# Optimization experiments

Measured on AMD Instinct MI355X. Metric: run time of the kernel, lower is better.

The kernel has to match this reference:

```python
import jax, jax.numpy as jnp
import numpy as np

TQ, TV, TA = 40, 64, 40
B = 2048
D = 1280          # per-stream feature dim; 4*D == 10*EMBED
EMBED = 512
EPS = 1e-5


def setup_inputs() -> dict:
    key = jax.random.key(0)
    ks = jax.random.split(key, 10)
    q  = jax.random.normal(ks[0], (TQ, B, D), jnp.float32)
    vq = jax.random.normal(ks[1], (TV, B, D), jnp.float32)
    a  = jax.random.normal(ks[2], (TA, B, D), jnp.float32)
    va = jax.random.normal(ks[3], (TV, B, D), jnp.float32)
    qlen = jax.random.randint(ks[4], (B,), 1, TQ + 1, dtype=jnp.int32)
    alen = jax.random.randint(ks[5], (B,), 1, TA + 1, dtype=jnp.int32)
    # classifier params (xavier-ish init)
    W1 = jax.random.normal(ks[6], (4 * D, EMBED), jnp.float32) * (2.0 / (4 * D + EMBED)) ** 0.5
    b1 = jnp.zeros((EMBED,), jnp.float32)
    gamma = jnp.ones((EMBED,), jnp.float32)
    beta = jnp.zeros((EMBED,), jnp.float32)
    W2 = jax.random.normal(ks[7], (EMBED, 1), jnp.float32) * (2.0 / (EMBED + 1)) ** 0.5
    b2 = jnp.zeros((1,), jnp.float32)
    return dict(question_embedding_v=q, visual_embedding_qu=vq,
                answer_embedding_v_expand=a, visual_embedding_an_expand=va,
                W1=W1, b1=b1, gamma=gamma, beta=beta, W2=W2, b2=b2,
                question_len=qlen, answers_len=alen)


def _masked_mean(x, lens):
    # x: [T, B, D], lens: [B] -> mean over first lens[j] timesteps per sample -> [B, D]
    T = x.shape[0]
    mask = (jnp.arange(T)[:, None] < lens[None, :]).astype(x.dtype)  # [T, B]
    return jnp.einsum('tbd,tb->bd', x, mask) / lens.astype(x.dtype)[:, None]


def reference(question_embedding_v, visual_embedding_qu,
              answer_embedding_v_expand, visual_embedding_an_expand,
              W1, b1, gamma, beta, W2, b2,
              question_len, answers_len):
    q  = _masked_mean(question_embedding_v, question_len)          # [B, D]
    vq = visual_embedding_qu.mean(axis=0)                          # [B, D]
    a  = _masked_mean(answer_embedding_v_expand, answers_len)      # [B, D]
    va = visual_embedding_an_expand.mean(axis=0)                   # [B, D]
    feat = jnp.concatenate([q, vq, a, va], axis=1)                 # [B, 4D] = [B, 10*EMBED]
    # Dropout is identity in eval/reference; BatchNorm1d uses batch stats (training mode).
    h = jax.nn.elu(feat @ W1 + b1)                                 # [B, EMBED]
    mu = h.mean(axis=0)
    var = h.var(axis=0)                                            # biased, like torch BN
    h = (h - mu) * jax.lax.rsqrt(var + EPS) * gamma + beta
    return h @ W2 + b2                                             # [B, 1]
```

## Files before the change

kernel.cpp:

```cpp
#include <hip/hip_runtime.h>
#include <hip/hip_bf16.h>

typedef __attribute__((ext_vector_type(8))) short bf16x8;
typedef __attribute__((ext_vector_type(4))) float f32x4;

#define NB 2048
#define ND 1280
#define NK 5120
#define NE 512

static __device__ inline unsigned short f2bf(float x) {
    union { float f; unsigned u; } c; c.f = x;
    unsigned r = c.u + 0x7FFFu + ((c.u >> 16) & 1u);
    return (unsigned short)(r >> 16);
}

__global__ __launch_bounds__(256) void reduce_kernel(
    const float4* __restrict__ q, const float4* __restrict__ vq,
    const float4* __restrict__ aa, const float4* __restrict__ va,
    const int* __restrict__ qlen, const int* __restrict__ alen,
    ushort4* __restrict__ feat)
{
    const int tid = blockIdx.x * 256 + threadIdx.x;
    const int per_seg = NB * (ND / 4);
    const int seg = tid / per_seg;
    const int r = tid - seg * per_seg;
    const int b = r / (ND / 4);
    const int ch = r - b * (ND / 4);

    const float4* src;
    int len;
    if (seg == 0)      { src = q;  len = qlen[b]; }
    else if (seg == 1) { src = vq; len = 64; }
    else if (seg == 2) { src = aa; len = alen[b]; }
    else               { src = va; len = 64; }

    const long base = (long)b * (ND / 4) + ch;
    const long stride = (long)NB * (ND / 4);

    float4 acc = make_float4(0.f, 0.f, 0.f, 0.f);
    #pragma unroll 4
    for (int t = 0; t < len; ++t) {
        float4 v = src[base + (long)t * stride];
        acc.x += v.x; acc.y += v.y; acc.z += v.z; acc.w += v.w;
    }
    const float inv = 1.0f / (float)len;
    ushort4 o;
    o.x = f2bf(acc.x * inv);
    o.y = f2bf(acc.y * inv);
    o.z = f2bf(acc.z * inv);
    o.w = f2bf(acc.w * inv);
    feat[(long)b * (NK / 4) + seg * (ND / 4) + ch] = o;
}

__global__ __launch_bounds__(256) void w1t_kernel(
    const float* __restrict__ W1, unsigned short* __restrict__ w1t)
{
    __shared__ unsigned short lds[32][33];
    const int bid = blockIdx.x;
    const int kb = (bid >> 4) * 32;
    const int nb = (bid & 15) * 32;
    const int tx = threadIdx.x & 31;
    const int ty = threadIdx.x >> 5;
    #pragma unroll
    for (int i = 0; i < 4; ++i) {
        int k = kb + ty + i * 8;
        lds[ty + i * 8][tx] = f2bf(W1[(long)k * NE + nb + tx]);
    }
    __syncthreads();
    #pragma unroll
    for (int i = 0; i < 4; ++i) {
        int n = nb + ty + i * 8;
        w1t[(long)n * NK + kb + tx] = lds[tx][ty + i * 8];
    }
}

__global__ __launch_bounds__(256) void gemm_kernel(
    const unsigned short* __restrict__ feat, const unsigned short* __restrict__ w1t,
    float* __restrict__ hpart)
{
    __shared__ int4 As[64 * 9];
    __shared__ int4 Bs[64 * 9];

    const int bid = blockIdx.x;
    const int tile = bid & 255;
    const int s = bid >> 8;
    const int m0 = (tile >> 3) << 6;
    const int n0 = (tile & 7) << 6;
    const int kbeg = s * (NK / 4);

    const int t = threadIdx.x;
    const int l = t & 63;
    const int w = t >> 6;
    const int wm = (w >> 1) * 32;
    const int wn = (w & 1) * 32;
    const int srow = t >> 3;
    const int scol = t & 7;

    f32x4 acc[2][2] = {};

    for (int k0 = kbeg; k0 < kbeg + NK / 4; k0 += 64) {
        const unsigned short* Ag = feat + (long)(m0 + srow) * NK + k0 + scol * 8;
        const unsigned short* Bg = w1t + (long)(n0 + srow) * NK + k0 + scol * 8;
        int4 a0 = *(const int4*)Ag;
        int4 a1 = *(const int4*)(Ag + 32L * NK);
        int4 b0 = *(const int4*)Bg;
        int4 b1v = *(const int4*)(Bg + 32L * NK);
        As[srow * 9 + scol] = a0;
        As[(srow + 32) * 9 + scol] = a1;
        Bs[srow * 9 + scol] = b0;
        Bs[(srow + 32) * 9 + scol] = b1v;
        __syncthreads();
        #pragma unroll
        for (int kk = 0; kk < 2; ++kk) {
            const int kc = kk * 4 + (l >> 4);
            bf16x8 af0 = *(const bf16x8*)&As[(wm + (l & 15)) * 9 + kc];
            bf16x8 af1 = *(const bf16x8*)&As[(wm + 16 + (l & 15)) * 9 + kc];
            bf16x8 bf0 = *(const bf16x8*)&Bs[(wn + (l & 15)) * 9 + kc];
            bf16x8 bf1 = *(const bf16x8*)&Bs[(wn + 16 + (l & 15)) * 9 + kc];
            acc[0][0] = __builtin_amdgcn_mfma_f32_16x16x32_bf16(af0, bf0, acc[0][0], 0, 0, 0);
            acc[0][1] = __builtin_amdgcn_mfma_f32_16x16x32_bf16(af0, bf1, acc[0][1], 0, 0, 0);
            acc[1][0] = __builtin_amdgcn_mfma_f32_16x16x32_bf16(af1, bf0, acc[1][0], 0, 0, 0);
            acc[1][1] = __builtin_amdgcn_mfma_f32_16x16x32_bf16(af1, bf1, acc[1][1], 0, 0, 0);
        }
        __syncthreads();
    }

    float* hp = hpart + (long)s * NB * NE;
    const int rbase = m0 + wm + ((l >> 4) << 2);
    const int cbase = n0 + wn + (l & 15);
    #pragma unroll
    for (int mi = 0; mi < 2; ++mi)
        #pragma unroll
        for (int ni = 0; ni < 2; ++ni)
            #pragma unroll
            for (int rr = 0; rr < 4; ++rr)
                hp[(long)(rbase + mi * 16 + rr) * NE + cbase + ni * 16] = acc[mi][ni][rr];
}

__global__ __launch_bounds__(256) void combine_kernel(
    const float* __restrict__ hpart, const float* __restrict__ b1,
    float* __restrict__ h, float* __restrict__ part1, float* __restrict__ part2)
{
    const int blk = blockIdx.x;
    const int t = threadIdx.x;
    const int c = t * 2;
    const float bx = b1[c], by = b1[c + 1];
    float s1x = 0.f, s1y = 0.f, s2x = 0.f, s2y = 0.f;
    const float2* hp = (const float2*)hpart;
    float2* h2 = (float2*)h;
    const long SL = (long)NB * NE / 2;
    for (int i = 0; i < 32; ++i) {
        long row = (long)blk * 32 + i;
        long idx = row * (NE / 2) + t;
        float2 v0 = hp[idx];
        float2 v1 = hp[idx + SL];
        float2 v2 = hp[idx + 2 * SL];
        float2 v3 = hp[idx + 3 * SL];
        float hx = v0.x + v1.x + v2.x + v3.x + bx;
        float hy = v0.y + v1.y + v2.y + v3.y + by;
        hx = hx > 0.f ? hx : expm1f(hx);
        hy = hy > 0.f ? hy : expm1f(hy);
        h2[idx] = make_float2(hx, hy);
        s1x += hx; s2x += hx * hx;
        s1y += hy; s2y += hy * hy;
    }
    float2* p1 = (float2*)part1;
    float2* p2 = (float2*)part2;
    p1[blk * (NE / 2) + t] = make_float2(s1x, s1y);
    p2[blk * (NE / 2) + t] = make_float2(s2x, s2y);
}

__global__ __launch_bounds__(512) void finalize_kernel(
    const float* __restrict__ part1, const float* __restrict__ part2,
    const float* __restrict__ gamma, const float* __restrict__ beta,
    const float* __restrict__ W2, const float* __restrict__ b2,
    float* __restrict__ coefA, float* __restrict__ cst)
{
    const int e = threadIdx.x;
    float s1 = 0.f, s2 = 0.f;
    for (int i = 0; i < 64; ++i) {
        s1 += part1[i * NE + e];
        s2 += part2[i * NE + e];
    }
    const float mu = s1 * (1.0f / NB);
    const float var = s2 * (1.0f / NB) - mu * mu;
    const float rs = rsqrtf(var + 1e-5f);
    const float g = gamma[e], w = W2[e];
    coefA[e] = rs * g * w;
    float term = (beta[e] - mu * rs * g) * w;
    __shared__ float red[512];
    red[e] = term;
    __syncthreads();
    for (int off = 256; off > 0; off >>= 1) {
        if (e < off) red[e] += red[e + off];
        __syncthreads();
    }
    if (e == 0) cst[0] = red[0] + b2[0];
}

__global__ __launch_bounds__(256) void out_kernel(
    const float* __restrict__ h, const float* __restrict__ coefA,
    const float* __restrict__ cst, float* __restrict__ out)
{
    const int w = threadIdx.x >> 6;
    const int l = threadIdx.x & 63;
    const int row = blockIdx.x * 4 + w;
    const float4* h4 = (const float4*)(h + (long)row * NE);
    const float4* c4 = (const float4*)coefA;
    float4 x0 = h4[l * 2], x1 = h4[l * 2 + 1];
    float4 c0 = c4[l * 2], c1 = c4[l * 2 + 1];
    float dot = x0.x * c0.x + x0.y * c0.y + x0.z * c0.z + x0.w * c0.w
              + x1.x * c1.x + x1.y * c1.y + x1.z * c1.z + x1.w * c1.w;
    #pragma unroll
    for (int off = 32; off > 0; off >>= 1) dot += __shfl_down(dot, off);
    if (l == 0) out[row] = dot + cst[0];
}

extern "C" void kernel_launch(void* const* d_in, const int* in_sizes, int n_in,
                              void* d_out, int out_size, void* d_ws, size_t ws_size,
                              hipStream_t stream)
{
    const float* q    = (const float*)d_in[0];
    const float* vq   = (const float*)d_in[1];
    const float* aa   = (const float*)d_in[2];
    const float* va   = (const float*)d_in[3];
    const float* W1   = (const float*)d_in[4];
    const float* b1   = (const float*)d_in[5];
    const float* gam  = (const float*)d_in[6];
    const float* bet  = (const float*)d_in[7];
    const float* W2   = (const float*)d_in[8];
    const float* b2   = (const float*)d_in[9];
    const int* qlen   = (const int*)d_in[10];
    const int* alen   = (const int*)d_in[11];
    float* out = (float*)d_out;

    char* ws = (char*)d_ws;
    unsigned short* feat = (unsigned short*)ws;
    unsigned short* w1t  = (unsigned short*)(ws + 20971520);
    float* hbuf          = (float*)(ws + 26214400);
    float* hpart         = (float*)(ws + 30408704);
    float* part1         = (float*)(ws + 47185920);
    float* part2         = (float*)(ws + 47316992);
    float* coefA         = (float*)(ws + 47448064);
    float* cst           = (float*)(ws + 47450112);

    reduce_kernel<<<10240, 256, 0, stream>>>(
        (const float4*)q, (const float4*)vq, (const float4*)aa, (const float4*)va,
        qlen, alen, (ushort4*)feat);

    w1t_kernel<<<2560, 256, 0, stream>>>(W1, w1t);

    gemm_kernel<<<1024, 256, 0, stream>>>(feat, w1t, hpart);

    combine_kernel<<<64, 256, 0, stream>>>(hpart, b1, hbuf, part1, part2);

    finalize_kernel<<<1, 512, 0, stream>>>(part1, part2, gam, bet, W2, b2, coefA, cst);

    out_kernel<<<512, 256, 0, stream>>>(hbuf, coefA, cst, out);
}
```

Before: 392.8 us.

## Fuse BN finalize into output kernel, atomically accumulate stats, widen reduce per-thread work

The reduce kernel now has each thread accumulate two float4 columns, which halves the grid. It also fully specialises the fixed-length (64) visual streams so their loop can be unrolled. The combine kernel runs on 256 blocks of 8 rows instead of 64 blocks of 32 rows, and pushes its per-column sums and sums of squares into a global buffer with atomics. The w1t kernel zeroes that buffer beforehand. The single-block finalize kernel is removed, and every output block now recomputes the BN coefficients into LDS itself. This drops one launch and a serial single-block step, at the cost of redundant coefficient work per block and nondeterministic float atomic ordering.

```diff
diff --git a/kernel.cpp b/kernel.cpp
--- a/kernel.cpp
+++ b/kernel.cpp
@@ -22,40 +22,59 @@
     ushort4* __restrict__ feat)
 {
     const int tid = blockIdx.x * 256 + threadIdx.x;
-    const int per_seg = NB * (ND / 4);
+    const int per_seg = NB * 160;
     const int seg = tid / per_seg;
     const int r = tid - seg * per_seg;
-    const int b = r / (ND / 4);
-    const int ch = r - b * (ND / 4);
-
-    const float4* src;
-    int len;
-    if (seg == 0)      { src = q;  len = qlen[b]; }
-    else if (seg == 1) { src = vq; len = 64; }
-    else if (seg == 2) { src = aa; len = alen[b]; }
-    else               { src = va; len = 64; }
-
-    const long base = (long)b * (ND / 4) + ch;
-    const long stride = (long)NB * (ND / 4);
-
-    float4 acc = make_float4(0.f, 0.f, 0.f, 0.f);
-    #pragma unroll 4
-    for (int t = 0; t < len; ++t) {
-        float4 v = src[base + (long)t * stride];
-        acc.x += v.x; acc.y += v.y; acc.z += v.z; acc.w += v.w;
-    }
-    const float inv = 1.0f / (float)len;
-    ushort4 o;
-    o.x = f2bf(acc.x * inv);
-    o.y = f2bf(acc.y * inv);
-    o.z = f2bf(acc.z * inv);
-    o.w = f2bf(acc.w * inv);
-    feat[(long)b * (NK / 4) + seg * (ND / 4) + ch] = o;
+    const int b = r / 160;
+    const int ch = r - b * 160;
+
+    const long base = (long)b * 320 + ch;
+    const long stride = (long)NB * 320;
+
+    float4 a0 = make_float4(0.f, 0.f, 0.f, 0.f);
+    float4 a1 = make_float4(0.f, 0.f, 0.f, 0.f);
+    float inv;
+
+    if (seg == 1 || seg == 3) {
+        const float4* src = (seg == 1) ? vq : va;
+        #pragma unroll 8
+        for (int t = 0; t < 64; ++t) {
+            float4 v0 = src[base + (long)t * stride];
+            float4 v1 = src[base + 160 + (long)t * stride];
+            a0.x += v0.x; a0.y += v0.y; a0.z += v0.z; a0.w += v0.w;
+            a1.x += v1.x; a1.y += v1.y; a1.z += v1.z; a1.w += v1.w;
+        }
+        inv = 1.0f / 64.0f;
+    } else {
+        const float4* src = (seg == 0) ? q : aa;
+        const int len = (seg == 0) ? qlen[b] : alen[b];
+        #pragma unroll 4
+        for (int t = 0; t < len; ++t) {
+            float4 v0 = src[base + (long)t * stride];
+            float4 v1 = src[base + 160 + (long)t * stride];
+            a0.x += v0.x; a0.y += v0.y; a0.z += v0.z; a0.w += v0.w;
+            a1.x += v1.x; a1.y += v1.y; a1.z += v1.z; a1.w += v1.w;
+        }
+        inv = 1.0f / (float)len;
+    }
+
+    ushort4 o0, o1;
+    o0.x = f2bf(a0.x * inv); o0.y = f2bf(a0.y * inv);
+    o0.z = f2bf(a0.z * inv); o0.w = f2bf(a0.w * inv);
+    o1.x = f2bf(a1.x * inv); o1.y = f2bf(a1.y * inv);
+    o1.z = f2bf(a1.z * inv); o1.w = f2bf(a1.w * inv);
+    const long fb = (long)b * (NK / 4) + seg * 320 + ch;
+    feat[fb] = o0;
+    feat[fb + 160] = o1;
 }
 
 __global__ __launch_bounds__(256) void w1t_kernel(
-    const float* __restrict__ W1, unsigned short* __restrict__ w1t)
-{
+    const float* __restrict__ W1, unsigned short* __restrict__ w1t,
+    float* __restrict__ s1s2)
+{
+    if (blockIdx.x == 0) {
+        ((float4*)s1s2)[threadIdx.x] = make_float4(0.f, 0.f, 0.f, 0.f);
+    }
     __shared__ unsigned short lds[32][33];
     const int bid = blockIdx.x;
     const int kb = (bid >> 4) * 32;
@@ -140,7 +159,7 @@
 
 __global__ __launch_bounds__(256) void combine_kernel(
     const float* __restrict__ hpart, const float* __restrict__ b1,
-    float* __restrict__ h, float* __restrict__ part1, float* __restrict__ part2)
+    float* __restrict__ h, float* __restrict__ s1s2)
 {
     const int blk = blockIdx.x;
     const int t = threadIdx.x;
@@ -150,8 +169,9 @@
     const float2* hp = (const float2*)hpart;
     float2* h2 = (float2*)h;
     const long SL = (long)NB * NE / 2;
-    for (int i = 0; i < 32; ++i) {
-        long row = (long)blk * 32 + i;
+    #pragma unroll
+    for (int i = 0; i < 8; ++i) {
+        long row = (long)blk * 8 + i;
         long idx = row * (NE / 2) + t;
         float2 v0 = hp[idx];
         float2 v1 = hp[idx + SL];
@@ -165,56 +185,56 @@
         s1x += hx; s2x += hx * hx;
         s1y += hy; s2y += hy * hy;
     }
-    float2* p1 = (float2*)part1;
-    float2* p2 = (float2*)part2;
-    p1[blk * (NE / 2) + t] = make_float2(s1x, s1y);
-    p2[blk * (NE / 2) + t] = make_float2(s2x, s2y);
-}
-
-__global__ __launch_bounds__(512) void finalize_kernel(
-    const float* __restrict__ part1, const float* __restrict__ part2,
+    unsafeAtomicAdd(&s1s2[c], s1x);
+    unsafeAtomicAdd(&s1s2[c + 1], s1y);
+    unsafeAtomicAdd(&s1s2[NE + c], s2x);
+    unsafeAtomicAdd(&s1s2[NE + c + 1], s2y);
+}
+
+__global__ __launch_bounds__(256) void out_kernel(
+    const float* __restrict__ h, const float* __restrict__ s1s2,
     const float* __restrict__ gamma, const float* __restrict__ beta,
     const float* __restrict__ W2, const float* __restrict__ b2,
-    float* __restrict__ coefA, float* __restrict__ cst)
-{
-    const int e = threadIdx.x;
-    float s1 = 0.f, s2 = 0.f;
-    for (int i = 0; i < 64; ++i) {
-        s1 += part1[i * NE + e];
-        s2 += part2[i * NE + e];
-    }
-    const float mu = s1 * (1.0f / NB);
-    const float var = s2 * (1.0f / NB) - mu * mu;
-    const float rs = rsqrtf(var + 1e-5f);
-    const float g = gamma[e], w = W2[e];
-    coefA[e] = rs * g * w;
-    float term = (beta[e] - mu * rs * g) * w;
-    __shared__ float red[512];
-    red[e] = term;
+    float* __restrict__ out)
+{
+    __shared__ float coef[NE];
+    __shared__ float red[256];
+    const int t = threadIdx.x;
+
+    float term = 0.f;
+    #pragma unroll
+    for (int i = 0; i < 2; ++i) {
+        const int e = t + i * 256;
+        const float s1 = s1s2[e];
+        const float s2 = s1s2[NE + e];
+        const float mu = s1 * (1.0f / NB);
+        const float var = s2 * (1.0f / NB) - mu * mu;
+        const float rs = rsqrtf(var + 1e-5f);
+        const float g = gamma[e], wv = W2[e];
+        coef[e] = rs * g * wv;
+        term += (beta[e] - mu * rs * g) * wv;
+    }
+    red[t] = term;
     __syncthreads();
-    for (int off = 256; off > 0; off >>= 1) {
-        if (e < off) red[e] += red[e + off];
+    #pragma unroll
+    for (int off = 128; off > 0; off >>= 1) {
+        if (t < off) red[t] += red[t + off];
         __syncthreads();
     }
-    if (e == 0) cst[0] = red[0] + b2[0];
-}
-
-__global__ __launch_bounds__(256) void out_kernel(
-    const float* __restrict__ h, const float* __restrict__ coefA,
-    const float* __restrict__ cst, float* __restrict__ out)
-{
-    const int w = threadIdx.x >> 6;
-    const int l = threadIdx.x & 63;
+    const float cst = red[0] + b2[0];
+
+    const int w = t >> 6;
+    const int l = t & 63;
     const int row = blockIdx.x * 4 + w;
     const float4* h4 = (const float4*)(h + (long)row * NE);
-    const float4* c4 = (const float4*)coefA;
     float4 x0 = h4[l * 2], x1 = h4[l * 2 + 1];
-    float4 c0 = c4[l * 2], c1 = c4[l * 2 + 1];
+    float4 c0 = *(const float4*)&coef[l * 8];
+    float4 c1 = *(const float4*)&coef[l * 8 + 4];
     float dot = x0.x * c0.x + x0.y * c0.y + x0.z * c0.z + x0.w * c0.w
               + x1.x * c1.x + x1.y * c1.y + x1.z * c1.z + x1.w * c1.w;
     #pragma unroll
     for (int off = 32; off > 0; off >>= 1) dot += __shfl_down(dot, off);
-    if (l == 0) out[row] = dot + cst[0];
+    if (l == 0) out[row] = dot + cst;
 }
 
 extern "C" void kernel_launch(void* const* d_in, const int* in_sizes, int n_in,
@@ -240,22 +260,17 @@
     unsigned short* w1t  = (unsigned short*)(ws + 20971520);
     float* hbuf          = (float*)(ws + 26214400);
     float* hpart         = (float*)(ws + 30408704);
-    float* part1         = (float*)(ws + 47185920);
-    float* part2         = (float*)(ws + 47316992);
-    float* coefA         = (float*)(ws + 47448064);
-    float* cst           = (float*)(ws + 47450112);
-
-    reduce_kernel<<<10240, 256, 0, stream>>>(
+    float* s1s2          = (float*)(ws + 47185920);
+
+    reduce_kernel<<<5120, 256, 0, stream>>>(
         (const float4*)q, (const float4*)vq, (const float4*)aa, (const float4*)va,
         qlen, alen, (ushort4*)feat);
 
-    w1t_kernel<<<2560, 256, 0, stream>>>(W1, w1t);
+    w1t_kernel<<<2560, 256, 0, stream>>>(W1, w1t, s1s2);
 
     gemm_kernel<<<1024, 256, 0, stream>>>(feat, w1t, hpart);
 
-    combine_kernel<<<64, 256, 0, stream>>>(hpart, b1, hbuf, part1, part2);
-
-    finalize_kernel<<<1, 512, 0, stream>>>(part1, part2, gam, bet, W2, b2, coefA, cst);
-
-    out_kernel<<<512, 256, 0, stream>>>(hbuf, coefA, cst, out);
-}
+    combine_kernel<<<256, 256, 0, stream>>>(hpart, b1, hbuf, s1s2);
+
+    out_kernel<<<512, 256, 0, stream>>>(hbuf, s1s2, gam, bet, W2, b2, out);
+}
```

Result: no change. 398.0 us (+1.3%).
